# Performance work log

Hardware: AMD Instinct MI355X
Metric: run time of the kernel (lower is better)

## Reference

```python
import jax, jax.numpy as jnp
import numpy as np

COLLAPSE_FRAC = 4  # collapse F // 4 lowest-weight faces (target_size = 3/4 * F)


def setup_inputs() -> dict:
    key = jax.random.key(0)
    k1, k2, k3 = jax.random.split(key, 3)
    B, F, C, K = 8, 8192, 256, 4
    features = jax.random.normal(k1, (B, F, C), dtype=jnp.float32)
    adjacency = jax.random.randint(k2, (B, F, 3), 0, F).astype(jnp.int32)
    ring_k = jax.random.randint(k3, (B, F, K), 0, F).astype(jnp.int32)
    return {"features": features, "adjacency": adjacency, "ring_k": ring_k}


def _pool(features, adjacency, ring_k):
    # features:  [B, F, C] float   per-face features
    # adjacency: [B, F, 3] int     3 neighboring faces of each triangle
    # ring_k:    [B, F, K] int     k-ring neighborhood used for collapse weights
    B, F, C = features.shape
    K = ring_k.shape[-1]
    # ring-aggregated saliency weight per face (compute_weights analogue)
    rf = jnp.take_along_axis(
        features, ring_k.reshape(B, F * K)[:, :, None], axis=1
    ).reshape(B, F, K, C)                      # [B, F, K, C]
    w = jnp.linalg.norm(rf.mean(axis=2), axis=-1)  # [B, F]

    # select lowest-weight faces to collapse (idx/sorted analogue)
    P = F // COLLAPSE_FRAC
    _, collapse_idx = jax.lax.top_k(-w, P)      # [B, P]

    # gather the 3 region neighbors and the collapsed face features
    neighbors = jnp.take_along_axis(adjacency, collapse_idx[:, :, None], axis=1)  # [B, P, 3]
    cf = jnp.take_along_axis(features, collapse_idx[:, :, None], axis=1)          # [B, P, C]

    # scatter collapsed-face features into their 3 adjacent faces (update_features analogue)
    offs = (jnp.arange(B, dtype=jnp.int32) * F)[:, None, None]   # [B, 1, 1]
    seg = (neighbors + offs).reshape(-1)                          # [B*P*3]
    vals = jnp.broadcast_to(cf[:, :, None, :] / 3.0, (B, P, 3, C)).reshape(-1, C)
    scat = jax.ops.segment_sum(vals, seg, num_segments=B * F).reshape(B, F, C)
    cnt = jax.ops.segment_sum(
        jnp.ones(seg.shape, jnp.float32), seg, num_segments=B * F
    ).reshape(B, F, 1)
    merged = (features + scat) / (1.0 + cnt)

    # erase collapsed faces (erased / update_faces analogue; static shape, mask instead of compaction)
    erase_flat = (collapse_idx + offs[:, :, 0]).reshape(-1)
    keep = (
        jnp.ones((B * F,), jnp.float32).at[erase_flat].set(0.0).reshape(B, F, 1)
    )
    return merged * keep


def reference(features, adjacency, ring_k):
    return _pool(features, adjacency, ring_k)
```

## Files before the change

kernel.cpp:

```cpp
#include <hip/hip_runtime.h>
#include <stdint.h>

#define B 8
#define F 8192
#define C 256
#define K 4
#define P (F / 4)
#define CAP 16
#define NB 4096
#define BF (B * F)
#define CCAP 4096

typedef float f32x4 __attribute__((ext_vector_type(4)));

__device__ __forceinline__ int binOf(float v, float lo, float scale) {
    int bin = (int)((v - lo) * scale);
    return bin < 0 ? 0 : (bin > NB - 1 ? NB - 1 : bin);
}

__global__ __launch_bounds__(256) void kW(const float* __restrict__ feat,
                                          const int* __restrict__ ring,
                                          float* __restrict__ w,
                                          int* __restrict__ cnt,
                                          int* __restrict__ flag) {
    const int b     = blockIdx.x & 7;
    const int inner = blockIdx.x >> 3;
    const int wid   = b * F + inner * 4 + (threadIdx.x >> 6);
    const int lane  = threadIdx.x & 63;

    const int rbase = wid * K;
    const int r0 = ring[rbase + 0], r1 = ring[rbase + 1];
    const int r2 = ring[rbase + 2], r3 = ring[rbase + 3];
    const float4* f4 = (const float4*)feat;
    const size_t base = (size_t)b * F;
    const int    CW   = C / 4;
    const float4 v0 = f4[(base + r0) * CW + lane];
    const float4 v1 = f4[(base + r1) * CW + lane];
    const float4 v2 = f4[(base + r2) * CW + lane];
    const float4 v3 = f4[(base + r3) * CW + lane];

    float4 a;
    a.x = (v0.x + v1.x) + (v2.x + v3.x);
    a.y = (v0.y + v1.y) + (v2.y + v3.y);
    a.z = (v0.z + v1.z) + (v2.z + v3.z);
    a.w = (v0.w + v1.w) + (v2.w + v3.w);
    float s = (a.x * a.x + a.y * a.y + a.z * a.z + a.w * a.w) * 0.0625f;
#pragma unroll
    for (int off = 32; off > 0; off >>= 1) s += __shfl_down(s, off, 64);
    if (lane == 0) {
        w[wid]    = s;
        cnt[wid]  = 0;
        flag[wid] = 0;
    }
}

__global__ __launch_bounds__(1024) void kHT(const float* __restrict__ w,
                                            const int* __restrict__ adj,
                                            int* __restrict__ tbin,
                                            unsigned int* __restrict__ lsb,
                                            int* __restrict__ flag,
                                            int* __restrict__ cnt,
                                            int* __restrict__ srcs) {
    __shared__ int h[NB];
    __shared__ unsigned long long carr[CCAP];
    __shared__ unsigned int redmn[16], redmx[16];
    __shared__ int wsum[16], woff[16];
    __shared__ unsigned int slo, shi;
    __shared__ int sT, sR, scnt;
    const int b = blockIdx.x, t = threadIdx.x;
    const int lane = t & 63, wv = t >> 6;

    if (t == 0) scnt = 0;

    float val[8];
    unsigned int mn = 0xFFFFFFFFu, mx = 0u;
#pragma unroll
    for (int k = 0; k < 8; ++k) {
        val[k] = w[b * F + t + k * 1024];
        const unsigned int u = __float_as_uint(val[k]);
        mn = mn < u ? mn : u;
        mx = mx > u ? mx : u;
    }
#pragma unroll
    for (int off = 32; off > 0; off >>= 1) {
        const unsigned int o1 = __shfl_xor(mn, off, 64); mn = mn < o1 ? mn : o1;
        const unsigned int o2 = __shfl_xor(mx, off, 64); mx = mx > o2 ? mx : o2;
    }
    if (lane == 0) { redmn[wv] = mn; redmx[wv] = mx; }
    for (int i = t; i < NB; i += 1024) h[i] = 0;
    __syncthreads();
    if (t == 0) {
        unsigned int a = redmn[0], c = redmx[0];
        for (int i = 1; i < 16; ++i) {
            a = a < redmn[i] ? a : redmn[i];
            c = c > redmx[i] ? c : redmx[i];
        }
        slo = a; shi = c;
    }
    __syncthreads();
    const unsigned int lob = slo, hib = shi;
    const float lo    = __uint_as_float(lob);
    const float hi    = __uint_as_float(hib);
    const float scale = (float)(NB - 2) / fmaxf(hi - lo, 1e-30f);

#pragma unroll
    for (int k = 0; k < 8; ++k) atomicAdd(&h[binOf(val[k], lo, scale)], 1);
    __syncthreads();

    int s = 0;
#pragma unroll
    for (int i = 0; i < 4; ++i) s += h[t * 4 + i];
    int incl = s;
#pragma unroll
    for (int off = 1; off < 64; off <<= 1) {
        const int u = __shfl_up(incl, off, 64);
        if (lane >= off) incl += u;
    }
    if (lane == 63) wsum[wv] = incl;
    __syncthreads();
    if (t < 16) {
        const int v = wsum[t];
        int iv = v;
#pragma unroll
        for (int off = 1; off < 16; off <<= 1) {
            const int u = __shfl_up(iv, off, 64);
            if (t >= off) iv += u;
        }
        woff[t] = iv - v;
    }
    __syncthreads();
    const int inclT = incl + woff[wv];
    const int exclT = inclT - s;
    if (P - 1 >= exclT && P - 1 < inclT) {
        int c = exclT;
#pragma unroll
        for (int i = 0; i < 4; ++i) {
            const int bin = t * 4 + i;
            const int hv  = h[bin];
            if (P - 1 < c + hv) { sT = bin; sR = P - c; break; }
            c += hv;
        }
    }
    if (t == 0) {
        lsb[b * 2 + 0] = lob;
        lsb[b * 2 + 1] = hib;
    }
    __syncthreads();
    const int T = sT, R = sR;
    if (t == 0) tbin[b] = T;

#pragma unroll
    for (int k = 0; k < 8; ++k) {
        if (binOf(val[k], lo, scale) == T) {
            const int pos = atomicAdd(&scnt, 1);
            if (pos < CCAP)
                carr[pos] = ((unsigned long long)__float_as_uint(val[k]) << 32) |
                            (uint32_t)(t + k * 1024);
        }
    }
    __syncthreads();
    const int n = scnt < CCAP ? scnt : CCAP;
    for (int i = t; i < n; i += 1024) {
        const unsigned long long my = carr[i];
        int rank = 0;
        for (int j = 0; j < n; ++j) rank += (carr[j] < my) ? 1 : 0;
        if (rank < R) {
            const int tt = b * F + (int)(uint32_t)my;
            flag[tt] = 1;
#pragma unroll
            for (int j = 0; j < 3; ++j) {
                const int nb   = adj[(size_t)tt * 3 + j];
                const int tgt  = b * F + nb;
                const int slot = atomicAdd(&cnt[tgt], 1);
                if (slot < CAP) srcs[(size_t)tgt * CAP + slot] = tt;
            }
        }
    }
}

__global__ __launch_bounds__(256) void kFL(const float* __restrict__ w,
                                           const int* __restrict__ adj,
                                           const unsigned int* __restrict__ lsb,
                                           const int* __restrict__ tbin,
                                           int* __restrict__ flag,
                                           int* __restrict__ cnt,
                                           int* __restrict__ srcs) {
    const int t = blockIdx.x * 256 + threadIdx.x;
    const int b = t >> 13;
    const float lo    = __uint_as_float(lsb[b * 2 + 0]);
    const float hi    = __uint_as_float(lsb[b * 2 + 1]);
    const float scale = (float)(NB - 2) / fmaxf(hi - lo, 1e-30f);

    const float v = w[t];
    if (binOf(v, lo, scale) < tbin[b]) {
        flag[t] = 1;
#pragma unroll
        for (int j = 0; j < 3; ++j) {
            const int n    = adj[(size_t)t * 3 + j];
            const int tgt  = b * F + n;
            const int slot = atomicAdd(&cnt[tgt], 1);
            if (slot < CAP) srcs[(size_t)tgt * CAP + slot] = t;
        }
    }
}

__global__ __launch_bounds__(256) void kG(const float* __restrict__ feat,
                                          const int* __restrict__ cnt,
                                          const int* __restrict__ flag,
                                          const int* __restrict__ srcs,
                                          float* __restrict__ out) {
    const int b     = blockIdx.x & 7;
    const int inner = blockIdx.x >> 3;
    const int wid   = b * F + inner * 4 + (threadIdx.x >> 6);
    const int lane  = threadIdx.x & 63;
    f32x4* drow = (f32x4*)(out + (size_t)wid * C);

    if (flag[wid]) {
        f32x4 z = {0.f, 0.f, 0.f, 0.f};
        __builtin_nontemporal_store(z, &drow[lane]);
        return;
    }
    const int m  = cnt[wid];
    const int mm = m < CAP ? m : CAP;

    const int sidx = (lane < CAP) ? srcs[(size_t)wid * CAP + lane] : 0;

    float4 acc = ((const float4*)(feat + (size_t)wid * C))[lane];
    const float inv3 = 1.0f / 3.0f;
    for (int i = 0; i < mm; ++i) {
        const int s = __shfl(sidx, i, 64);
        const float4 v = ((const float4*)(feat + (size_t)s * C))[lane];
        acc.x += v.x * inv3; acc.y += v.y * inv3;
        acc.z += v.z * inv3; acc.w += v.w * inv3;
    }
    const float inv = 1.0f / (1.0f + (float)m);
    f32x4 r;
    r.x = acc.x * inv; r.y = acc.y * inv;
    r.z = acc.z * inv; r.w = acc.w * inv;
    __builtin_nontemporal_store(r, &drow[lane]);
}

extern "C" void kernel_launch(void* const* d_in, const int* in_sizes, int n_in,
                              void* d_out, int out_size, void* d_ws, size_t ws_size,
                              hipStream_t stream) {
    const float* feat = (const float*)d_in[0];
    const int*   adj  = (const int*)d_in[1];
    const int*   ring = (const int*)d_in[2];
    float* out = (float*)d_out;

    float* w    = (float*)d_ws;
    int*   cnt  = (int*)(w + BF);
    int*   flag = cnt + BF;
    int*   srcs = flag + BF;
    int*   tbin = srcs + (size_t)BF * CAP;
    unsigned int* lsb = (unsigned int*)(tbin + B);

    kW  <<<BF / 4, 256, 0, stream>>>(feat, ring, w, cnt, flag);
    kHT <<<B, 1024, 0, stream>>>(w, adj, tbin, lsb, flag, cnt, srcs);
    kFL <<<BF / 256, 256, 0, stream>>>(w, adj, lsb, tbin, flag, cnt, srcs);
    kG  <<<BF / 4, 256, 0, stream>>>(feat, cnt, flag, srcs, out);
}
```

Before: 156.5 us.

## Fuse histogram threshold and flagging kernels with redundant per-block histogram

```diff
diff --git a/kernel.cpp b/kernel.cpp
--- a/kernel.cpp
+++ b/kernel.cpp
@@ -9,7 +9,7 @@
 #define CAP 16
 #define NB 4096
 #define BF (B * F)
-#define CCAP 4096
+#define CCAP 1024
 
 typedef float f32x4 __attribute__((ext_vector_type(4)));
 
@@ -54,29 +54,31 @@
     }
 }
 
-__global__ __launch_bounds__(1024) void kHT(const float* __restrict__ w,
-                                            const int* __restrict__ adj,
-                                            int* __restrict__ tbin,
-                                            unsigned int* __restrict__ lsb,
-                                            int* __restrict__ flag,
-                                            int* __restrict__ cnt,
-                                            int* __restrict__ srcs) {
+__global__ __launch_bounds__(256) void kFS(const float* __restrict__ w,
+                                           const int* __restrict__ adj,
+                                           int* __restrict__ flag,
+                                           int* __restrict__ cnt,
+                                           int* __restrict__ srcs) {
     __shared__ int h[NB];
     __shared__ unsigned long long carr[CCAP];
-    __shared__ unsigned int redmn[16], redmx[16];
-    __shared__ int wsum[16], woff[16];
+    __shared__ unsigned int redmn[4], redmx[4];
+    __shared__ int wsum[4];
     __shared__ unsigned int slo, shi;
     __shared__ int sT, sR, scnt;
-    const int b = blockIdx.x, t = threadIdx.x;
+    const int g    = blockIdx.x;
+    const int b    = g >> 5;
+    const int gg   = g & 31;
+    const int t    = threadIdx.x;
     const int lane = t & 63, wv = t >> 6;
 
     if (t == 0) scnt = 0;
-
-    float val[8];
+    for (int i = t; i < NB; i += 256) h[i] = 0;
+
+    float val[32];
     unsigned int mn = 0xFFFFFFFFu, mx = 0u;
 #pragma unroll
-    for (int k = 0; k < 8; ++k) {
-        val[k] = w[b * F + t + k * 1024];
+    for (int k = 0; k < 32; ++k) {
+        val[k] = w[b * F + k * 256 + t];
         const unsigned int u = __float_as_uint(val[k]);
         mn = mn < u ? mn : u;
         mx = mx > u ? mx : u;
@@ -87,29 +89,27 @@
         const unsigned int o2 = __shfl_xor(mx, off, 64); mx = mx > o2 ? mx : o2;
     }
     if (lane == 0) { redmn[wv] = mn; redmx[wv] = mx; }
-    for (int i = t; i < NB; i += 1024) h[i] = 0;
     __syncthreads();
     if (t == 0) {
         unsigned int a = redmn[0], c = redmx[0];
-        for (int i = 1; i < 16; ++i) {
+        for (int i = 1; i < 4; ++i) {
             a = a < redmn[i] ? a : redmn[i];
             c = c > redmx[i] ? c : redmx[i];
         }
         slo = a; shi = c;
     }
     __syncthreads();
-    const unsigned int lob = slo, hib = shi;
-    const float lo    = __uint_as_float(lob);
-    const float hi    = __uint_as_float(hib);
+    const float lo    = __uint_as_float(slo);
+    const float hi    = __uint_as_float(shi);
     const float scale = (float)(NB - 2) / fmaxf(hi - lo, 1e-30f);
 
 #pragma unroll
-    for (int k = 0; k < 8; ++k) atomicAdd(&h[binOf(val[k], lo, scale)], 1);
+    for (int k = 0; k < 32; ++k) atomicAdd(&h[binOf(val[k], lo, scale)], 1);
     __syncthreads();
 
     int s = 0;
 #pragma unroll
-    for (int i = 0; i < 4; ++i) s += h[t * 4 + i];
+    for (int i = 0; i < 16; ++i) s += h[t * 16 + i];
     int incl = s;
 #pragma unroll
     for (int off = 1; off < 64; off <<= 1) {
@@ -118,88 +118,63 @@
     }
     if (lane == 63) wsum[wv] = incl;
     __syncthreads();
-    if (t < 16) {
-        const int v = wsum[t];
-        int iv = v;
-#pragma unroll
-        for (int off = 1; off < 16; off <<= 1) {
-            const int u = __shfl_up(iv, off, 64);
-            if (t >= off) iv += u;
-        }
-        woff[t] = iv - v;
-    }
-    __syncthreads();
-    const int inclT = incl + woff[wv];
+    int add = 0;
+    for (int i = 0; i < wv; ++i) add += wsum[i];
+    const int inclT = incl + add;
     const int exclT = inclT - s;
     if (P - 1 >= exclT && P - 1 < inclT) {
         int c = exclT;
 #pragma unroll
-        for (int i = 0; i < 4; ++i) {
-            const int bin = t * 4 + i;
+        for (int i = 0; i < 16; ++i) {
+            const int bin = t * 16 + i;
             const int hv  = h[bin];
             if (P - 1 < c + hv) { sT = bin; sR = P - c; break; }
             c += hv;
         }
     }
-    if (t == 0) {
-        lsb[b * 2 + 0] = lob;
-        lsb[b * 2 + 1] = hib;
-    }
     __syncthreads();
     const int T = sT, R = sR;
-    if (t == 0) tbin[b] = T;
-
-#pragma unroll
-    for (int k = 0; k < 8; ++k) {
-        if (binOf(val[k], lo, scale) == T) {
-            const int pos = atomicAdd(&scnt, 1);
-            if (pos < CCAP)
-                carr[pos] = ((unsigned long long)__float_as_uint(val[k]) << 32) |
-                            (uint32_t)(t + k * 1024);
-        }
-    }
-    __syncthreads();
-    const int n = scnt < CCAP ? scnt : CCAP;
-    for (int i = t; i < n; i += 1024) {
-        const unsigned long long my = carr[i];
-        int rank = 0;
-        for (int j = 0; j < n; ++j) rank += (carr[j] < my) ? 1 : 0;
-        if (rank < R) {
-            const int tt = b * F + (int)(uint32_t)my;
-            flag[tt] = 1;
-#pragma unroll
-            for (int j = 0; j < 3; ++j) {
-                const int nb   = adj[(size_t)tt * 3 + j];
-                const int tgt  = b * F + nb;
-                const int slot = atomicAdd(&cnt[tgt], 1);
-                if (slot < CAP) srcs[(size_t)tgt * CAP + slot] = tt;
-            }
-        }
-    }
-}
-
-__global__ __launch_bounds__(256) void kFL(const float* __restrict__ w,
-                                           const int* __restrict__ adj,
-                                           const unsigned int* __restrict__ lsb,
-                                           const int* __restrict__ tbin,
-                                           int* __restrict__ flag,
-                                           int* __restrict__ cnt,
-                                           int* __restrict__ srcs) {
-    const int t = blockIdx.x * 256 + threadIdx.x;
-    const int b = t >> 13;
-    const float lo    = __uint_as_float(lsb[b * 2 + 0]);
-    const float hi    = __uint_as_float(lsb[b * 2 + 1]);
-    const float scale = (float)(NB - 2) / fmaxf(hi - lo, 1e-30f);
-
-    const float v = w[t];
-    if (binOf(v, lo, scale) < tbin[b]) {
-        flag[t] = 1;
+
+    const float myv = val[gg];
+    const int face  = b * F + gg * 256 + t;
+    if (binOf(myv, lo, scale) < T) {
+        flag[face] = 1;
 #pragma unroll
         for (int j = 0; j < 3; ++j) {
-            const int n    = adj[(size_t)t * 3 + j];
+            const int n    = adj[(size_t)face * 3 + j];
             const int tgt  = b * F + n;
             const int slot = atomicAdd(&cnt[tgt], 1);
-            if (slot < CAP) srcs[(size_t)tgt * CAP + slot] = t;
+            if (slot < CAP) srcs[(size_t)tgt * CAP + slot] = face;
+        }
+    }
+
+    if (gg == 0) {
+#pragma unroll
+        for (int k = 0; k < 32; ++k) {
+            if (binOf(val[k], lo, scale) == T) {
+                const int pos = atomicAdd(&scnt, 1);
+                if (pos < CCAP)
+                    carr[pos] = ((unsigned long long)__float_as_uint(val[k]) << 32) |
+                                (uint32_t)(k * 256 + t);
+            }
+        }
+        __syncthreads();
+        const int n = scnt < CCAP ? scnt : CCAP;
+        for (int i = t; i < n; i += 256) {
+            const unsigned long long my = carr[i];
+            int rank = 0;
+            for (int j = 0; j < n; ++j) rank += (carr[j] < my) ? 1 : 0;
+            if (rank < R) {
+                const int tt = b * F + (int)(uint32_t)my;
+                flag[tt] = 1;
+#pragma unroll
+                for (int j = 0; j < 3; ++j) {
+                    const int nb   = adj[(size_t)tt * 3 + j];
+                    const int tgt  = b * F + nb;
+                    const int slot = atomicAdd(&cnt[tgt], 1);
+                    if (slot < CAP) srcs[(size_t)tgt * CAP + slot] = tt;
+                }
+            }
         }
     }
 }
@@ -223,15 +198,16 @@
     const int m  = cnt[wid];
     const int mm = m < CAP ? m : CAP;
 
-    const int sidx = (lane < CAP) ? srcs[(size_t)wid * CAP + lane] : 0;
-
     float4 acc = ((const float4*)(feat + (size_t)wid * C))[lane];
-    const float inv3 = 1.0f / 3.0f;
-    for (int i = 0; i < mm; ++i) {
-        const int s = __shfl(sidx, i, 64);
-        const float4 v = ((const float4*)(feat + (size_t)s * C))[lane];
-        acc.x += v.x * inv3; acc.y += v.y * inv3;
-        acc.z += v.z * inv3; acc.w += v.w * inv3;
+    if (mm > 0) {
+        const int sidx = (lane < CAP) ? srcs[(size_t)wid * CAP + lane] : 0;
+        const float inv3 = 1.0f / 3.0f;
+        for (int i = 0; i < mm; ++i) {
+            const int s = __shfl(sidx, i, 64);
+            const float4 v = ((const float4*)(feat + (size_t)s * C))[lane];
+            acc.x += v.x * inv3; acc.y += v.y * inv3;
+            acc.z += v.z * inv3; acc.w += v.w * inv3;
+        }
     }
     const float inv = 1.0f / (1.0f + (float)m);
     f32x4 r;
@@ -252,11 +228,8 @@
     int*   cnt  = (int*)(w + BF);
     int*   flag = cnt + BF;
     int*   srcs = flag + BF;
-    int*   tbin = srcs + (size_t)BF * CAP;
-    unsigned int* lsb = (unsigned int*)(tbin + B);
 
     kW  <<<BF / 4, 256, 0, stream>>>(feat, ring, w, cnt, flag);
-    kHT <<<B, 1024, 0, stream>>>(w, adj, tbin, lsb, flag, cnt, srcs);
-    kFL <<<BF / 256, 256, 0, stream>>>(w, adj, lsb, tbin, flag, cnt, srcs);
+    kFS <<<BF / 256, 256, 0, stream>>>(w, adj, flag, cnt, srcs);
     kG  <<<BF / 4, 256, 0, stream>>>(feat, cnt, flag, srcs, out);
 }
```

New measurement: 156.6 us. Within noise of the previous version (+0.1%).
